# Performance work log

Hardware: AMD Instinct MI355X
Metric: run time of the kernel (lower is better)

Reference implementation:

```python
import jax, jax.numpy as jnp
import numpy as np

B, N, P_CTR, K = 16, 2048, 256, 32
H, W = 24, 80
INFEA = 64
MLP = [64, 128, 128, 256]
DIST = 0.5
EPS = 1e-5


def setup_inputs() -> dict:
    key = jax.random.key(0)
    ks = jax.random.split(key, 12)
    inp = {}
    inp['pc'] = jax.random.normal(ks[0], (B, 3, N), jnp.float32)
    inp['feat'] = jax.random.normal(ks[1], (B, INFEA, N), jnp.float32)
    inp['img1'] = jax.random.normal(ks[2], (B, MLP[0], H, W), jnp.float32)
    inp['img2'] = jax.random.normal(ks[3], (B, MLP[1], H, W), jnp.float32)
    inp['P'] = jax.random.normal(ks[4], (B, 3, 4), jnp.float32)
    inp['query_v1'] = jax.random.randint(ks[5], (B, N), 0, H * W, dtype=jnp.int32)
    inp['new_pc'] = jax.random.normal(ks[6], (B, 3, P_CTR), jnp.float32)
    dims = [INFEA + 3] + MLP  # conv chain: 67->64->128->128->256, 1x1 convs, no bias
    for i in range(4):
        fan_in = dims[i]
        inp[f'w{i+1}'] = jax.random.normal(ks[7 + i], (dims[i + 1], dims[i]), jnp.float32) * np.sqrt(2.0 / fan_in)
        inp[f'g{i+1}'] = jnp.ones((dims[i + 1],), jnp.float32)   # BN gamma, init 1
        inp[f'b{i+1}'] = jnp.zeros((dims[i + 1],), jnp.float32)  # BN beta, init 0
    return inp


def query_depth_point(pc, new_pc, dist, k):
    # depth (z-axis) ball query: pc (B,3,N), new_pc (B,3,P) -> idx (B,P,k) int32, num (B,P)
    dz = jnp.abs(pc[:, 2, None, :] - new_pc[:, 2, :, None])  # (B,P,N)
    mask = dz < dist
    num = jnp.sum(mask, axis=-1).astype(jnp.int32)           # neighbor count per center
    # stable argsort of ~mask puts valid indices first, in ascending original order
    order = jnp.argsort(jnp.logical_not(mask), axis=-1, stable=True)
    idx = order[..., :k]
    slot_valid = jnp.arange(k)[None, None, :] < jnp.minimum(num, k)[..., None]
    idx = jnp.where(slot_valid, idx, idx[..., :1])           # pad with first valid index
    return idx.astype(jnp.int32), num


def gather_ch(x, idx):
    # x (B,C,M), idx (B,L) -> (B,C,L)
    return jnp.take_along_axis(x, idx[:, None, :], axis=2)


def conv_bn_relu(x, w, g, b):
    # 1x1 conv (no bias) + BatchNorm2d (training-mode batch stats) + ReLU
    y = jnp.einsum('oc,bcnk->bonk', w, x)
    m = jnp.mean(y, axis=(0, 2, 3), keepdims=True)
    v = jnp.var(y, axis=(0, 2, 3), keepdims=True)
    y = (y - m) * jax.lax.rsqrt(v + EPS)
    y = y * g[None, :, None, None] + b[None, :, None, None]
    return jax.nn.relu(y)


def reference(pc, feat, img1, img2, P, query_v1, new_pc,
              w1, g1, b1, w2, g2, b2, w3, g3, b3, w4, g4, b4):
    idx, num = query_depth_point(pc, new_pc, DIST, K)       # (B,P,K), (B,P)
    idx_flat = idx.reshape(B, P_CTR * K)
    idx_rgb = jnp.take_along_axis(query_v1, idx_flat, axis=1)  # (B,P*K) pixel ids

    grouped_pc = gather_ch(pc, idx_flat).reshape(B, 3, P_CTR, K) - new_pc[:, :, :, None]
    grouped_feat = gather_ch(feat, idx_flat).reshape(B, INFEA, P_CTR, K)
    rgb1 = gather_ch(img1.reshape(B, MLP[0], H * W), idx_rgb).reshape(B, MLP[0], P_CTR, K)
    rgb2 = gather_ch(img2.reshape(B, MLP[1], H * W), idx_rgb).reshape(B, MLP[1], P_CTR, K)

    grouped = jnp.concatenate([grouped_pc, grouped_feat], axis=1)  # (B,67,P,K)
    pf = conv_bn_relu(grouped, w1, g1, b1)                         # (B,64,P,K)
    f1 = jnp.concatenate([pf, rgb1], axis=1)                       # (B,128,P,K)
    pf = conv_bn_relu(pf, w2, g2, b2)                              # (B,128,P,K)
    f2 = jnp.concatenate([pf, rgb2], axis=1)                       # (B,256,P,K)
    pf = conv_bn_relu(pf, w3, g3, b3)
    pf = conv_bn_relu(pf, w4, g4, b4)                              # (B,256,P,K)
    out = jnp.concatenate([f1, f2, pf], axis=1)                    # (B,640,P,K)
    valid = (num > 0).reshape(B, 1, P_CTR, 1).astype(out.dtype)
    return out * valid
```

## Files before the change

kernel.cpp:

```cpp
#include <hip/hip_runtime.h>
#include <hip/hip_fp16.h>

#define BB 16
#define NN 2048
#define PC 256
#define KK 32
#define HWS 1920
#define PT (BB*PC*KK)
#define EPSF 1e-5f

#define CH_IDXR 256
#define CH_IDX  257
#define CH_VAL  258
#define CH_FT   356
#define STATS_OFF ((size_t)259 << 13)

typedef _Float16 f16x8 __attribute__((ext_vector_type(8)));
typedef float    f32x4 __attribute__((ext_vector_type(4)));

__device__ __forceinline__ unsigned packh2(float lo, float hi) {
  unsigned a = (unsigned)__half_as_ushort(__float2half(lo));
  unsigned b = (unsigned)__half_as_ushort(__float2half(hi));
  return a | (b << 16);
}
__device__ __forceinline__ float h2lo(unsigned u) {
  return __half2float(__ushort_as_half((unsigned short)(u & 0xffffu)));
}
__device__ __forceinline__ float h2hi(unsigned u) {
  return __half2float(__ushort_as_half((unsigned short)(u >> 16)));
}

__global__ __launch_bounds__(256,2) void k_prep(
    const float* __restrict__ feat, float* out)
{
  __shared__ float tile[64][261];
  int tid = threadIdx.x;
  int b = blockIdx.x >> 3, n0 = (blockIdx.x & 7) << 8;
  #pragma unroll 8
  for (int c = 0; c < 64; c++)
    tile[c][tid] = feat[((size_t)b*64 + c)*NN + n0 + tid];
  __syncthreads();
  unsigned* ftw = (unsigned*)out + (((size_t)b*640 + CH_FT)<<13);
  #pragma unroll
  for (int e = tid; e < 256*32; e += 256) {
    int q = e & 31, nl = e >> 5;
    ftw[(size_t)(n0 + nl)*32 + q] = packh2(tile[2*q][nl], tile[2*q+1][nl]);
  }
}

template<bool WSC>
__global__ __launch_bounds__(256) void k_idx(
    const float* __restrict__ pc, const float* __restrict__ npc,
    const int* __restrict__ qv1, float* out, int* __restrict__ wsi)
{
  __shared__ int slots[4][KK];
  int tid = threadIdx.x;
  if (blockIdx.x < 5) {
    int i = blockIdx.x*256 + tid;
    if (i < 1152) out[STATS_OFF + i] = 0.0f;
  }
  int wl = tid >> 6, lane = tid & 63;
  int w = blockIdx.x*4 + wl;
  int b = w >> 8, p = w & 255;
  if (lane == 0) slots[wl][0] = 0;
  float zc = npc[(b*3+2)*PC + p];
  const float* pz = pc + ((size_t)b*3+2)*NN;
  int num = 0;
  for (int ci=0; ci<NN/64; ci++) {
    int n = ci*64 + lane;
    bool m = fabsf(pz[n] - zc) < 0.5f;
    unsigned long long mk = __ballot(m);
    if (m) {
      int rank = num + __popcll(mk & ((1ull<<lane)-1ull));
      if (rank < KK) slots[wl][rank] = n;
    }
    num += __popcll(mk);
  }
  __syncthreads();
  if (lane < KK) {
    int nj = (lane < num) ? slots[wl][lane] : slots[wl][0];
    size_t col = (size_t)p*KK + lane;
    int enc = (num > 0) ? qv1[b*NN + nj] : -1;
    ((int*)out)[(((size_t)b*640 + CH_IDX )<<13) + col] = nj;
    ((int*)out)[(((size_t)b*640 + CH_IDXR)<<13) + col] = enc;
    if constexpr (WSC) wsi[(size_t)b*8192 + col] = enc;
  }
  if (lane == 0)
    out[(((size_t)b*640 + CH_VAL)<<13) + (size_t)p*KK] = (num > 0) ? 1.0f : 0.0f;
}

#define THR 512
template<int CIN, int CINP, int COUT, int BOCH, int WVP, int WVO, int WFP, int WFO,
         int XMODE, int XBASE, int YMODE, int YBASE, int STIN, int STOUT,
         int SWZ, int QR, int PFB>
__global__ __launch_bounds__(THR,4) void k_mfma(
    const float* __restrict__ pc, const float* __restrict__ npc,
    const float* __restrict__ feat, const float* __restrict__ W,
    const float* __restrict__ g, const float* __restrict__ bv,
    float* out)
{
  __shared__ __align__(16) _Float16 xs[128*QR*2];
  __shared__ __align__(16) _Float16 ws[BOCH*QR*2];
  __shared__ float scs[128], shs[128];
  __shared__ int   idxl[128];
  __shared__ float redu[WVP*BOCH*2];

  int tid = threadIdx.x;
  int ptile = blockIdx.x;
  int b = ptile >> 6;
  int col0 = (ptile & 63) << 7;
  int och0 = blockIdx.y * BOCH;

  unsigned* xsw = (unsigned*)xs;
  unsigned* wsw = (unsigned*)ws;

  for (int e = tid; e < BOCH*QR; e += THR) {
    int o = e / QR, cq = e - o*QR;
    int c0 = 2*cq;
    float v0, v1;
    if constexpr (XMODE == 0) {
      int r0 = (c0   < 64) ? c0 + 3   : c0 - 64;
      int r1 = (c0+1 < 64) ? c0 + 4   : c0 + 1 - 64;
      v0 = (c0   < CIN) ? W[(size_t)(och0+o)*CIN + r0] : 0.f;
      v1 = (c0+1 < CIN) ? W[(size_t)(och0+o)*CIN + r1] : 0.f;
    } else {
      v0 = (c0   < CIN) ? W[(size_t)(och0+o)*CIN + c0]     : 0.f;
      v1 = (c0+1 < CIN) ? W[(size_t)(och0+o)*CIN + c0 + 1] : 0.f;
    }
    wsw[o*QR + cq] = packh2(v0, v1);
  }
  if constexpr (XMODE == 0) {
    if (tid < 128)
      idxl[tid] = ((const int*)out)[(((size_t)b*640 + CH_IDX)<<13) + col0 + tid];
  } else {
    const float* stin = out + STATS_OFF + STIN;
    for (int c = tid; c < CIN; c += THR) {
      float m   = stin[c] * (1.0f/PT);
      float var = stin[CIN+c]*(1.0f/PT) - m*m;
      float s = rsqrtf(var + EPSF) * g[c];
      scs[c] = s; shs[c] = bv[c] - m*s;
    }
  }
  __syncthreads();

  if constexpr (XMODE == 0) {
    constexpr int QG = CINP/2;
    const unsigned* ftw = (const unsigned*)out + (((size_t)b*640 + CH_FT)<<13);
    for (int e = tid; e < QG*128; e += THR) {
      int q = e % QG, pos = e / QG;
      int n = idxl[pos];
      unsigned u;
      if (q < 32) {
        u = ftw[(size_t)n*32 + q];
      } else if (q == 32) {
        int pcol = (col0 + pos) >> 5;
        float vx = pc[((size_t)b*3+0)*NN + n] - npc[(b*3+0)*PC + pcol];
        float vy = pc[((size_t)b*3+1)*NN + n] - npc[(b*3+1)*PC + pcol];
        u = packh2(vx, vy);
      } else if (q == 33) {
        int pcol = (col0 + pos) >> 5;
        float vz = pc[((size_t)b*3+2)*NN + n] - npc[(b*3+2)*PC + pcol];
        u = packh2(vz, 0.f);
      } else {
        u = 0u;
      }
      int qs = (((q>>2) ^ ((pos>>2) & SWZ)) << 2) | (q & 3);
      xsw[pos*QR + qs] = u;
    }
  } else {
    constexpr int QG = CIN/2;
    for (int e = tid; e < QG*32; e += THR) {
      int q = e >> 5, pg = e & 31;
      uint4 u = *(const uint4*)&((const unsigned*)out)[(((size_t)b*640 + XBASE + q)<<13) + col0 + pg*4];
      float s0 = scs[2*q], h0 = shs[2*q], s1 = scs[2*q+1], h1 = shs[2*q+1];
      unsigned uu[4] = {u.x, u.y, u.z, u.w};
      float lo_a[4], hi_a[4];
      #pragma unroll
      for (int j = 0; j < 4; j++) {
        float lo = fmaxf(fmaf(h2lo(uu[j]), s0, h0), 0.f);
        float hi = fmaxf(fmaf(h2hi(uu[j]), s1, h1), 0.f);
        lo_a[j] = lo; hi_a[j] = hi;
        int p = pg*4 + j;
        xsw[p*QR + ((((q>>2) ^ ((p>>2) & SWZ)) << 2) | (q & 3))] = packh2(lo, hi);
      }
      if constexpr (PFB >= 0) {
        float vv = out[(((size_t)b*640 + CH_VAL)<<13) + col0 + ((pg >> 3) << 5)];
        float4 L = {lo_a[0]*vv, lo_a[1]*vv, lo_a[2]*vv, lo_a[3]*vv};
        float4 Hh = {hi_a[0]*vv, hi_a[1]*vv, hi_a[2]*vv, hi_a[3]*vv};
        size_t pb = (((size_t)b*640 + PFB + 2*q)<<13) + col0 + pg*4;
        *(float4*)&out[pb]              = L;
        *(float4*)&out[pb + (1<<13)]    = Hh;
      }
    }
  }
  __syncthreads();

  int wv = tid >> 6, lane = tid & 63;
  int wp = wv % WVP, wo = wv / WVP;
  int lr = lane & 15, lg = lane >> 4;
  int prow0 = wp*(WFP*16), orow0 = wo*(WFO*16);

  f32x4 acc[WFP][WFO];
  const f32x4 zero4 = {0.f, 0.f, 0.f, 0.f};
  #pragma unroll
  for (int fp = 0; fp < WFP; fp++)
    #pragma unroll
    for (int fo = 0; fo < WFO; fo++) acc[fp][fo] = zero4;

  #pragma unroll
  for (int kc = 0; kc < CINP/32; kc++) {
    f16x8 af[WFP], bf[WFO];
    #pragma unroll
    for (int fp = 0; fp < WFP; fp++) {
      int row = prow0 + fp*16 + lr;
      int qb = (kc*4 + lg) ^ ((row>>2) & SWZ);
      af[fp] = *(const f16x8*)&xs[row*(QR*2) + qb*8];
    }
    #pragma unroll
    for (int fo = 0; fo < WFO; fo++) {
      int orow = orow0 + fo*16 + lr;
      bf[fo] = *(const f16x8*)&ws[orow*(QR*2) + kc*32 + lg*8];
    }
    #pragma unroll
    for (int fp = 0; fp < WFP; fp++)
      #pragma unroll
      for (int fo = 0; fo < WFO; fo++)
        acc[fp][fo] = __builtin_amdgcn_mfma_f32_16x16x32_f16(af[fp], bf[fo], acc[fp][fo], 0, 0, 0);
  }

  if constexpr (YMODE == 0) {
    #pragma unroll
    for (int fp = 0; fp < WFP; fp++) {
      int pos = col0 + prow0 + fp*16 + lg*4;
      #pragma unroll
      for (int fo = 0; fo < WFO; fo++) {
        int ochg = och0 + orow0 + fo*16 + lr;
        *(f32x4*)&out[(((size_t)b*640 + YBASE + ochg)<<13) + pos] = acc[fp][fo];
      }
    }
  } else {
    #pragma unroll
    for (int fp = 0; fp < WFP; fp++) {
      int pos = col0 + prow0 + fp*16 + lg*4;
      #pragma unroll
      for (int fo = 0; fo < WFO; fo++) {
        float pr0 = __shfl_xor(acc[fp][fo][0], 1);
        float pr1 = __shfl_xor(acc[fp][fo][1], 1);
        float pr2 = __shfl_xor(acc[fp][fo][2], 1);
        float pr3 = __shfl_xor(acc[fp][fo][3], 1);
        if (!(lane & 1)) {
          uint4 u;
          u.x = packh2(acc[fp][fo][0], pr0);
          u.y = packh2(acc[fp][fo][1], pr1);
          u.z = packh2(acc[fp][fo][2], pr2);
          u.w = packh2(acc[fp][fo][3], pr3);
          int qrow = (och0 + orow0 + fo*16 + lr) >> 1;
          *(uint4*)&((unsigned*)out)[(((size_t)b*640 + YBASE + qrow)<<13) + pos] = u;
        }
      }
    }
  }

  #pragma unroll
  for (int fo = 0; fo < WFO; fo++) {
    float s = 0.f, q2 = 0.f;
    #pragma unroll
    for (int fp = 0; fp < WFP; fp++)
      #pragma unroll
      for (int r = 0; r < 4; r++) { float v = acc[fp][fo][r]; s += v; q2 += v*v; }
    s  += __shfl_down(s, 32);  s  += __shfl_down(s, 16);
    q2 += __shfl_down(q2, 32); q2 += __shfl_down(q2, 16);
    if (lane < 16) {
      int oloc = orow0 + fo*16 + lane;
      redu[(wp*BOCH + oloc)*2]     = s;
      redu[(wp*BOCH + oloc)*2 + 1] = q2;
    }
  }
  __syncthreads();
  float* stg = out + STATS_OFF + STOUT;
  for (int i = tid; i < BOCH; i += THR) {
    float ss = 0.f, qq = 0.f;
    #pragma unroll
    for (int p = 0; p < WVP; p++) { ss += redu[(p*BOCH + i)*2]; qq += redu[(p*BOCH + i)*2 + 1]; }
    atomicAdd(&stg[och0 + i], ss);
    atomicAdd(&stg[COUT + och0 + i], qq);
  }
}

__global__ __launch_bounds__(256) void k_norm4(
    const float* __restrict__ g, const float* __restrict__ bv, float* out)
{
  __shared__ float sc[256], sh[256];
  int tid = threadIdx.x;
  const float* stin = out + STATS_OFF + 640;
  {
    float m   = stin[tid] * (1.0f/PT);
    float var = stin[256+tid]*(1.0f/PT) - m*m;
    float s = rsqrtf(var + EPSF) * g[tid];
    sc[tid] = s; sh[tid] = bv[tid] - m*s;
  }
  __syncthreads();
  int pos = blockIdx.x*256 + tid;
  int b = pos >> 13, rem = pos & 8191;
  float v = out[(((size_t)b*640 + CH_VAL)<<13) + (rem & ~31)];
  const unsigned* srcp = (const unsigned*)out + (((size_t)b*640 + 512)<<13) + rem;
  float* dstp = out + (((size_t)b*640 + 384)<<13) + rem;
  unsigned u[64];
  #pragma unroll
  for (int qi = 0; qi < 64; qi++) u[qi] = srcp[(size_t)(64+qi)<<13];
  #pragma unroll 8
  for (int qi = 0; qi < 64; qi++) {
    unsigned w = srcp[(size_t)qi<<13];
    dstp[(size_t)(2*qi)<<13]   = fmaxf(fmaf(h2lo(w), sc[2*qi],   sh[2*qi]),   0.f) * v;
    dstp[(size_t)(2*qi+1)<<13] = fmaxf(fmaf(h2hi(w), sc[2*qi+1], sh[2*qi+1]), 0.f) * v;
  }
  #pragma unroll 8
  for (int qi = 0; qi < 64; qi++) {
    dstp[(size_t)(128+2*qi)<<13]   = fmaxf(fmaf(h2lo(u[qi]), sc[128+2*qi],   sh[128+2*qi]),   0.f) * v;
    dstp[(size_t)(128+2*qi+1)<<13] = fmaxf(fmaf(h2hi(u[qi]), sc[128+2*qi+1], sh[128+2*qi+1]), 0.f) * v;
  }
}

__global__ __launch_bounds__(256) void k_rgb_lds(
    const float* __restrict__ img1, const float* __restrict__ img2,
    const int* __restrict__ wsi, float* out)
{
  __shared__ float ls[4][HWS];
  int tid = threadIdx.x;
  int b = blockIdx.x / 96, r = blockIdx.x % 96;
  int gq = r >> 1, half = r & 1;
  int gc0 = gq * 4;
  for (int e = tid; e < 4*(HWS/4); e += 256) {
    int c = e / (HWS/4), off = e % (HWS/4);
    int gc = gc0 + c;
    const float* src = (gc < 64) ? img1 + ((size_t)b*64 + gc)*HWS
                                 : img2 + ((size_t)b*128 + (gc-64))*HWS;
    *(float4*)&ls[c][off*4] = *(const float4*)&src[off*4];
  }
  __syncthreads();
  const int* idr = wsi + (size_t)b*8192;
  for (int pp = half*4096 + tid; pp < (half+1)*4096; pp += 256) {
    int enc = idr[pp];
    float v = (enc >= 0) ? 1.0f : 0.0f;
    int ir  = (enc >= 0) ? enc : 0;
    #pragma unroll
    for (int c = 0; c < 4; c++) {
      int gc = gc0 + c;
      int dch = (gc < 64) ? 64 + gc : 256 + (gc - 64);
      out[(((size_t)b*640 + dch)<<13) + pp] = ls[c][ir] * v;
    }
  }
}

__global__ __launch_bounds__(256) void k_rgb_fb(
    const float* __restrict__ img1, const float* __restrict__ img2, float* out)
{
  int tid = threadIdx.x;
  int pos = blockIdx.x*256 + tid;
  int b = pos >> 13, rem = pos & 8191;
  int enc = ((const int*)out)[(((size_t)b*640 + CH_IDXR)<<13) + rem];
  float v  = (enc >= 0) ? 1.0f : 0.0f;
  int  ir  = (enc >= 0) ? enc : 0;
  size_t o1 = (((size_t)b*640 + 64)<<13) + rem;
  const float* i1 = img1 + (size_t)b*64*HWS + ir;
  #pragma unroll 8
  for (int c=0;c<64;c++) out[o1 + ((size_t)c<<13)] = i1[(size_t)c*HWS] * v;
  size_t o2 = (((size_t)b*640 + 256)<<13) + rem;
  const float* i2 = img2 + (size_t)b*128*HWS + ir;
  #pragma unroll 8
  for (int c=0;c<128;c++) out[o2 + ((size_t)c<<13)] = i2[(size_t)c*HWS] * v;
}

extern "C" void kernel_launch(void* const* d_in, const int* in_sizes, int n_in,
                              void* d_out, int out_size, void* d_ws, size_t ws_size,
                              hipStream_t stream)
{
  const float* pc   = (const float*)d_in[0];
  const float* feat = (const float*)d_in[1];
  const float* img1 = (const float*)d_in[2];
  const float* img2 = (const float*)d_in[3];
  const int*   qv1  = (const int*)d_in[5];
  const float* npc  = (const float*)d_in[6];
  const float* w1 = (const float*)d_in[7];
  const float* g1 = (const float*)d_in[8];
  const float* b1 = (const float*)d_in[9];
  const float* w2 = (const float*)d_in[10];
  const float* g2 = (const float*)d_in[11];
  const float* b2 = (const float*)d_in[12];
  const float* w3 = (const float*)d_in[13];
  const float* g3 = (const float*)d_in[14];
  const float* b3 = (const float*)d_in[15];
  const float* w4 = (const float*)d_in[16];
  const float* g4 = (const float*)d_in[17];
  const float* b4 = (const float*)d_in[18];
  float* out = (float*)d_out;
  int*  wsi = (int*)d_ws;
  const bool use_ws = (d_ws != nullptr) && (ws_size >= (size_t)BB*8192*4);

  k_prep <<<128,256,0,stream>>>(feat, out);
  if (use_ws) k_idx<true ><<<1024,256,0,stream>>>(pc, npc, qv1, out, wsi);
  else        k_idx<false><<<1024,256,0,stream>>>(pc, npc, qv1, out, wsi);
  k_mfma<67,96,64,64,    2,4,4,1, 0,0,   1,324, 0,0,     0,48, -1>
      <<<dim3(1024,1),THR,0,stream>>>(pc,npc,feat,w1,g1,b1,out);
  k_mfma<64,64,128,128,  2,4,4,2, 1,324, 1,260, 0,128,   7,36, 0>
      <<<dim3(1024,1),THR,0,stream>>>(pc,npc,feat,w2,g1,b1,out);
  k_mfma<128,128,128,128,2,4,4,2, 1,260, 1,64,  128,384, 7,68, 128>
      <<<dim3(1024,1),THR,0,stream>>>(pc,npc,feat,w3,g2,b2,out);
  k_mfma<128,128,256,128,2,4,4,2, 1,64,  1,512, 384,640, 7,68, -1>
      <<<dim3(1024,2),THR,0,stream>>>(pc,npc,feat,w4,g3,b3,out);
  k_norm4<<<512,256,0,stream>>>(g4,b4,out);
  if (use_ws) k_rgb_lds<<<1536,256,0,stream>>>(img1, img2, wsi, out);
  else        k_rgb_fb <<<512,256,0,stream>>>(img1, img2, out);
}
```

Baseline: 654.6 us.

## Recompute final conv layer to fuse BN-ReLU output and drop norm kernel

Layer 4 now runs twice. The first pass only accumulates batch statistics. The second recomputes the GEMM and writes the normalized, ReLU'd, validity-masked fp32 output directly, which removes the fp16 intermediate round-trip and the separate k_norm4 kernel. In addition, each MFMA block now processes two point tiles with double-buffered LDS staging, keeps the fp16 weight fragments in registers instead of LDS, and the RGB gather kernel uses 512-thread blocks covering all positions. The trade is extra GEMM compute and a second read of the layer-4 input, plus higher register pressure from the register-resident weights.

```diff
diff --git a/kernel.cpp b/kernel.cpp
--- a/kernel.cpp
+++ b/kernel.cpp
@@ -8,6 +8,7 @@
 #define HWS 1920
 #define PT (BB*PC*KK)
 #define EPSF 1e-5f
+#define THR 512
 
 #define CH_IDXR 256
 #define CH_IDX  257
@@ -89,50 +90,56 @@
     out[(((size_t)b*640 + CH_VAL)<<13) + (size_t)p*KK] = (num > 0) ? 1.0f : 0.0f;
 }
 
-#define THR 512
 template<int CIN, int CINP, int COUT, int BOCH, int WVP, int WVO, int WFP, int WFO,
          int XMODE, int XBASE, int YMODE, int YBASE, int STIN, int STOUT,
-         int SWZ, int QR, int PFB>
+         int SWZ, int QR, int PFB, int TILES>
 __global__ __launch_bounds__(THR,4) void k_mfma(
     const float* __restrict__ pc, const float* __restrict__ npc,
-    const float* __restrict__ feat, const float* __restrict__ W,
+    const float* __restrict__ W,
     const float* __restrict__ g, const float* __restrict__ bv,
+    const float* __restrict__ go, const float* __restrict__ bo,
     float* out)
 {
-  __shared__ __align__(16) _Float16 xs[128*QR*2];
-  __shared__ __align__(16) _Float16 ws[BOCH*QR*2];
+  constexpr int KC = CINP/32;
+  __shared__ __align__(16) _Float16 xs[2][128*QR*2];
   __shared__ float scs[128], shs[128];
-  __shared__ int   idxl[128];
   __shared__ float redu[WVP*BOCH*2];
 
   int tid = threadIdx.x;
-  int ptile = blockIdx.x;
-  int b = ptile >> 6;
-  int col0 = (ptile & 63) << 7;
+  int tile0 = blockIdx.x * TILES;
+  int b = tile0 >> 6;
   int och0 = blockIdx.y * BOCH;
 
-  unsigned* xsw = (unsigned*)xs;
-  unsigned* wsw = (unsigned*)ws;
-
-  for (int e = tid; e < BOCH*QR; e += THR) {
-    int o = e / QR, cq = e - o*QR;
-    int c0 = 2*cq;
-    float v0, v1;
-    if constexpr (XMODE == 0) {
-      int r0 = (c0   < 64) ? c0 + 3   : c0 - 64;
-      int r1 = (c0+1 < 64) ? c0 + 4   : c0 + 1 - 64;
-      v0 = (c0   < CIN) ? W[(size_t)(och0+o)*CIN + r0] : 0.f;
-      v1 = (c0+1 < CIN) ? W[(size_t)(och0+o)*CIN + r1] : 0.f;
-    } else {
-      v0 = (c0   < CIN) ? W[(size_t)(och0+o)*CIN + c0]     : 0.f;
-      v1 = (c0+1 < CIN) ? W[(size_t)(och0+o)*CIN + c0 + 1] : 0.f;
-    }
-    wsw[o*QR + cq] = packh2(v0, v1);
-  }
-  if constexpr (XMODE == 0) {
-    if (tid < 128)
-      idxl[tid] = ((const int*)out)[(((size_t)b*640 + CH_IDX)<<13) + col0 + tid];
-  } else {
+  int wv = tid >> 6, lane = tid & 63;
+  int wp = wv % WVP, wo = wv / WVP;
+  int lr = lane & 15, lg = lane >> 4;
+  int prow0 = wp*(WFP*16), orow0 = wo*(WFO*16);
+
+  f16x8 bfr[KC][WFO];
+  #pragma unroll
+  for (int kc = 0; kc < KC; kc++)
+    #pragma unroll
+    for (int fo = 0; fo < WFO; fo++) {
+      int orow = och0 + orow0 + fo*16 + lr;
+      f16x8 tf;
+      if constexpr (XMODE == 0) {
+        #pragma unroll
+        for (int j = 0; j < 8; j++) {
+          int c = kc*32 + lg*8 + j;
+          int r = (c < 64) ? c + 3 : (c < 67 ? c - 64 : -1);
+          tf[j] = (_Float16)((r >= 0) ? W[(size_t)orow*CIN + r] : 0.f);
+        }
+      } else {
+        const float* wr = W + (size_t)orow*CIN + kc*32 + lg*8;
+        float4 w0 = *(const float4*)wr;
+        float4 w1 = *(const float4*)(wr + 4);
+        tf[0]=(_Float16)w0.x; tf[1]=(_Float16)w0.y; tf[2]=(_Float16)w0.z; tf[3]=(_Float16)w0.w;
+        tf[4]=(_Float16)w1.x; tf[5]=(_Float16)w1.y; tf[6]=(_Float16)w1.z; tf[7]=(_Float16)w1.w;
+      }
+      bfr[kc][fo] = tf;
+    }
+
+  if constexpr (XMODE == 1) {
     const float* stin = out + STATS_OFF + STIN;
     for (int c = tid; c < CIN; c += THR) {
       float m   = stin[c] * (1.0f/PT);
@@ -141,196 +148,194 @@
       scs[c] = s; shs[c] = bv[c] - m*s;
     }
   }
+  float osc_[WFO], osh_[WFO];
+  if constexpr (YMODE == 3) {
+    const float* sto = out + STATS_OFF + STOUT;
+    #pragma unroll
+    for (int fo = 0; fo < WFO; fo++) {
+      int och = och0 + orow0 + fo*16 + lr;
+      float m   = sto[och]*(1.0f/PT);
+      float var = sto[COUT+och]*(1.0f/PT) - m*m;
+      float s = rsqrtf(var + EPSF) * go[och];
+      osc_[fo] = s; osh_[fo] = bo[och] - m*s;
+    }
+  }
   __syncthreads();
 
-  if constexpr (XMODE == 0) {
-    constexpr int QG = CINP/2;
-    const unsigned* ftw = (const unsigned*)out + (((size_t)b*640 + CH_FT)<<13);
-    for (int e = tid; e < QG*128; e += THR) {
-      int q = e % QG, pos = e / QG;
-      int n = idxl[pos];
-      unsigned u;
-      if (q < 32) {
-        u = ftw[(size_t)n*32 + q];
-      } else if (q == 32) {
-        int pcol = (col0 + pos) >> 5;
-        float vx = pc[((size_t)b*3+0)*NN + n] - npc[(b*3+0)*PC + pcol];
-        float vy = pc[((size_t)b*3+1)*NN + n] - npc[(b*3+1)*PC + pcol];
-        u = packh2(vx, vy);
-      } else if (q == 33) {
-        int pcol = (col0 + pos) >> 5;
-        float vz = pc[((size_t)b*3+2)*NN + n] - npc[(b*3+2)*PC + pcol];
-        u = packh2(vz, 0.f);
-      } else {
-        u = 0u;
-      }
-      int qs = (((q>>2) ^ ((pos>>2) & SWZ)) << 2) | (q & 3);
-      xsw[pos*QR + qs] = u;
-    }
-  } else {
-    constexpr int QG = CIN/2;
-    for (int e = tid; e < QG*32; e += THR) {
-      int q = e >> 5, pg = e & 31;
-      uint4 u = *(const uint4*)&((const unsigned*)out)[(((size_t)b*640 + XBASE + q)<<13) + col0 + pg*4];
-      float s0 = scs[2*q], h0 = shs[2*q], s1 = scs[2*q+1], h1 = shs[2*q+1];
-      unsigned uu[4] = {u.x, u.y, u.z, u.w};
-      float lo_a[4], hi_a[4];
-      #pragma unroll
-      for (int j = 0; j < 4; j++) {
-        float lo = fmaxf(fmaf(h2lo(uu[j]), s0, h0), 0.f);
-        float hi = fmaxf(fmaf(h2hi(uu[j]), s1, h1), 0.f);
-        lo_a[j] = lo; hi_a[j] = hi;
-        int p = pg*4 + j;
-        xsw[p*QR + ((((q>>2) ^ ((p>>2) & SWZ)) << 2) | (q & 3))] = packh2(lo, hi);
-      }
-      if constexpr (PFB >= 0) {
-        float vv = out[(((size_t)b*640 + CH_VAL)<<13) + col0 + ((pg >> 3) << 5)];
-        float4 L = {lo_a[0]*vv, lo_a[1]*vv, lo_a[2]*vv, lo_a[3]*vv};
-        float4 Hh = {hi_a[0]*vv, hi_a[1]*vv, hi_a[2]*vv, hi_a[3]*vv};
-        size_t pb = (((size_t)b*640 + PFB + 2*q)<<13) + col0 + pg*4;
-        *(float4*)&out[pb]              = L;
-        *(float4*)&out[pb + (1<<13)]    = Hh;
-      }
-    }
-  }
+  auto STAGE = [&](int t) {
+    int col0t = ((tile0 + t) & 63) << 7;
+    unsigned* xw = (unsigned*)xs[t & 1];
+    if constexpr (XMODE == 0) {
+      int posl = tid & 127;
+      int qb0  = tid >> 7;
+      int n = ((const int*)out)[(((size_t)b*640 + CH_IDX)<<13) + col0t + posl];
+      const unsigned* ftw = (const unsigned*)out + (((size_t)b*640 + CH_FT)<<13);
+      int pcol = (col0t + posl) >> 5;
+      #pragma unroll
+      for (int k = 0; k < 12; k++) {
+        int q = qb0 + k*4;
+        unsigned u;
+        if (q < 32) {
+          u = ftw[(size_t)n*32 + q];
+        } else if (q == 32) {
+          float vx = pc[((size_t)b*3+0)*NN + n] - npc[(b*3+0)*PC + pcol];
+          float vy = pc[((size_t)b*3+1)*NN + n] - npc[(b*3+1)*PC + pcol];
+          u = packh2(vx, vy);
+        } else if (q == 33) {
+          float vz = pc[((size_t)b*3+2)*NN + n] - npc[(b*3+2)*PC + pcol];
+          u = packh2(vz, 0.f);
+        } else u = 0u;
+        int qs = (((q>>2) ^ ((posl>>2) & SWZ)) << 2) | (q & 3);
+        xw[posl*QR + qs] = u;
+      }
+    } else {
+      #pragma unroll
+      for (int k = 0; k < CIN/32; k++) {
+        int e = tid + k*THR;
+        int q = e >> 5, pg = e & 31;
+        uint4 u = *(const uint4*)&((const unsigned*)out)[(((size_t)b*640 + XBASE + q)<<13) + col0t + pg*4];
+        float s0 = scs[2*q], h0 = shs[2*q], s1 = scs[2*q+1], h1 = shs[2*q+1];
+        unsigned uu[4] = {u.x, u.y, u.z, u.w};
+        float lo_a[4], hi_a[4];
+        #pragma unroll
+        for (int j = 0; j < 4; j++) {
+          lo_a[j] = fmaxf(fmaf(h2lo(uu[j]), s0, h0), 0.f);
+          hi_a[j] = fmaxf(fmaf(h2hi(uu[j]), s1, h1), 0.f);
+          int p = pg*4 + j;
+          xw[p*QR + ((((q>>2) ^ ((p>>2) & SWZ)) << 2) | (q & 3))] = packh2(lo_a[j], hi_a[j]);
+        }
+        if constexpr (PFB >= 0) {
+          float vv = out[(((size_t)b*640 + CH_VAL)<<13) + col0t + ((pg >> 3) << 5)];
+          float4 L  = {lo_a[0]*vv, lo_a[1]*vv, lo_a[2]*vv, lo_a[3]*vv};
+          float4 Hh = {hi_a[0]*vv, hi_a[1]*vv, hi_a[2]*vv, hi_a[3]*vv};
+          size_t pb = (((size_t)b*640 + PFB + 2*q)<<13) + col0t + pg*4;
+          *(float4*)&out[pb]           = L;
+          *(float4*)&out[pb + (1<<13)] = Hh;
+        }
+      }
+    }
+  };
+
+  STAGE(0);
   __syncthreads();
 
-  int wv = tid >> 6, lane = tid & 63;
-  int wp = wv % WVP, wo = wv / WVP;
-  int lr = lane & 15, lg = lane >> 4;
-  int prow0 = wp*(WFP*16), orow0 = wo*(WFO*16);
-
-  f32x4 acc[WFP][WFO];
-  const f32x4 zero4 = {0.f, 0.f, 0.f, 0.f};
+  float ssum[WFO], ssq[WFO];
   #pragma unroll
-  for (int fp = 0; fp < WFP; fp++)
-    #pragma unroll
-    for (int fo = 0; fo < WFO; fo++) acc[fp][fo] = zero4;
+  for (int fo = 0; fo < WFO; fo++) { ssum[fo] = 0.f; ssq[fo] = 0.f; }
 
   #pragma unroll
-  for (int kc = 0; kc < CINP/32; kc++) {
-    f16x8 af[WFP], bf[WFO];
-    #pragma unroll
-    for (int fp = 0; fp < WFP; fp++) {
-      int row = prow0 + fp*16 + lr;
-      int qb = (kc*4 + lg) ^ ((row>>2) & SWZ);
-      af[fp] = *(const f16x8*)&xs[row*(QR*2) + qb*8];
-    }
+  for (int t = 0; t < TILES; t++) {
+    int col0t = ((tile0 + t) & 63) << 7;
+    const _Float16* xb = xs[t & 1];
+
+    f32x4 acc[WFP][WFO];
+    const f32x4 zero4 = {0.f, 0.f, 0.f, 0.f};
+    #pragma unroll
+    for (int fp = 0; fp < WFP; fp++)
+      #pragma unroll
+      for (int fo = 0; fo < WFO; fo++) acc[fp][fo] = zero4;
+
+    #pragma unroll
+    for (int kc = 0; kc < KC; kc++) {
+      f16x8 af[WFP];
+      #pragma unroll
+      for (int fp = 0; fp < WFP; fp++) {
+        int row = prow0 + fp*16 + lr;
+        int qb = (kc*4 + lg) ^ ((row>>2) & SWZ);
+        af[fp] = *(const f16x8*)&xb[row*(QR*2) + qb*8];
+      }
+      #pragma unroll
+      for (int fp = 0; fp < WFP; fp++)
+        #pragma unroll
+        for (int fo = 0; fo < WFO; fo++)
+          acc[fp][fo] = __builtin_amdgcn_mfma_f32_16x16x32_f16(af[fp], bfr[kc][fo], acc[fp][fo], 0, 0, 0);
+    }
+
+    if constexpr (YMODE == 1) {
+      #pragma unroll
+      for (int fp = 0; fp < WFP; fp++) {
+        int pos = col0t + prow0 + fp*16 + lg*4;
+        #pragma unroll
+        for (int fo = 0; fo < WFO; fo++) {
+          float pr0 = __shfl_xor(acc[fp][fo][0], 1);
+          float pr1 = __shfl_xor(acc[fp][fo][1], 1);
+          float pr2 = __shfl_xor(acc[fp][fo][2], 1);
+          float pr3 = __shfl_xor(acc[fp][fo][3], 1);
+          if (!(lane & 1)) {
+            uint4 u;
+            u.x = packh2(acc[fp][fo][0], pr0); u.y = packh2(acc[fp][fo][1], pr1);
+            u.z = packh2(acc[fp][fo][2], pr2); u.w = packh2(acc[fp][fo][3], pr3);
+            int qrow = (och0 + orow0 + fo*16 + lr) >> 1;
+            *(uint4*)&((unsigned*)out)[(((size_t)b*640 + YBASE + qrow)<<13) + pos] = u;
+          }
+        }
+      }
+    } else if constexpr (YMODE == 3) {
+      #pragma unroll
+      for (int fp = 0; fp < WFP; fp++) {
+        int pos = col0t + prow0 + fp*16 + lg*4;
+        float v = out[(((size_t)b*640 + CH_VAL)<<13) + (pos & ~31)];
+        #pragma unroll
+        for (int fo = 0; fo < WFO; fo++) {
+          int och = och0 + orow0 + fo*16 + lr;
+          f32x4 wv;
+          #pragma unroll
+          for (int r = 0; r < 4; r++)
+            wv[r] = fmaxf(fmaf(acc[fp][fo][r], osc_[fo], osh_[fo]), 0.f) * v;
+          *(f32x4*)&out[(((size_t)b*640 + YBASE + och)<<13) + pos] = wv;
+        }
+      }
+    }
+
+    if constexpr (YMODE != 3) {
+      #pragma unroll
+      for (int fo = 0; fo < WFO; fo++)
+        #pragma unroll
+        for (int fp = 0; fp < WFP; fp++)
+          #pragma unroll
+          for (int r = 0; r < 4; r++) {
+            float v = acc[fp][fo][r];
+            ssum[fo] += v; ssq[fo] += v*v;
+          }
+    }
+
+    if (t + 1 < TILES) STAGE(t + 1);
+    __syncthreads();
+  }
+
+  if constexpr (YMODE != 3) {
     #pragma unroll
     for (int fo = 0; fo < WFO; fo++) {
-      int orow = orow0 + fo*16 + lr;
-      bf[fo] = *(const f16x8*)&ws[orow*(QR*2) + kc*32 + lg*8];
-    }
-    #pragma unroll
-    for (int fp = 0; fp < WFP; fp++)
-      #pragma unroll
-      for (int fo = 0; fo < WFO; fo++)
-        acc[fp][fo] = __builtin_amdgcn_mfma_f32_16x16x32_f16(af[fp], bf[fo], acc[fp][fo], 0, 0, 0);
-  }
-
-  if constexpr (YMODE == 0) {
-    #pragma unroll
-    for (int fp = 0; fp < WFP; fp++) {
-      int pos = col0 + prow0 + fp*16 + lg*4;
-      #pragma unroll
-      for (int fo = 0; fo < WFO; fo++) {
-        int ochg = och0 + orow0 + fo*16 + lr;
-        *(f32x4*)&out[(((size_t)b*640 + YBASE + ochg)<<13) + pos] = acc[fp][fo];
-      }
-    }
-  } else {
-    #pragma unroll
-    for (int fp = 0; fp < WFP; fp++) {
-      int pos = col0 + prow0 + fp*16 + lg*4;
-      #pragma unroll
-      for (int fo = 0; fo < WFO; fo++) {
-        float pr0 = __shfl_xor(acc[fp][fo][0], 1);
-        float pr1 = __shfl_xor(acc[fp][fo][1], 1);
-        float pr2 = __shfl_xor(acc[fp][fo][2], 1);
-        float pr3 = __shfl_xor(acc[fp][fo][3], 1);
-        if (!(lane & 1)) {
-          uint4 u;
-          u.x = packh2(acc[fp][fo][0], pr0);
-          u.y = packh2(acc[fp][fo][1], pr1);
-          u.z = packh2(acc[fp][fo][2], pr2);
-          u.w = packh2(acc[fp][fo][3], pr3);
-          int qrow = (och0 + orow0 + fo*16 + lr) >> 1;
-          *(uint4*)&((unsigned*)out)[(((size_t)b*640 + YBASE + qrow)<<13) + pos] = u;
-        }
-      }
-    }
-  }
-
-  #pragma unroll
-  for (int fo = 0; fo < WFO; fo++) {
-    float s = 0.f, q2 = 0.f;
-    #pragma unroll
-    for (int fp = 0; fp < WFP; fp++)
-      #pragma unroll
-      for (int r = 0; r < 4; r++) { float v = acc[fp][fo][r]; s += v; q2 += v*v; }
-    s  += __shfl_down(s, 32);  s  += __shfl_down(s, 16);
-    q2 += __shfl_down(q2, 32); q2 += __shfl_down(q2, 16);
-    if (lane < 16) {
-      int oloc = orow0 + fo*16 + lane;
-      redu[(wp*BOCH + oloc)*2]     = s;
-      redu[(wp*BOCH + oloc)*2 + 1] = q2;
-    }
-  }
-  __syncthreads();
-  float* stg = out + STATS_OFF + STOUT;
-  for (int i = tid; i < BOCH; i += THR) {
-    float ss = 0.f, qq = 0.f;
-    #pragma unroll
-    for (int p = 0; p < WVP; p++) { ss += redu[(p*BOCH + i)*2]; qq += redu[(p*BOCH + i)*2 + 1]; }
-    atomicAdd(&stg[och0 + i], ss);
-    atomicAdd(&stg[COUT + och0 + i], qq);
-  }
-}
-
-__global__ __launch_bounds__(256) void k_norm4(
-    const float* __restrict__ g, const float* __restrict__ bv, float* out)
-{
-  __shared__ float sc[256], sh[256];
-  int tid = threadIdx.x;
-  const float* stin = out + STATS_OFF + 640;
-  {
-    float m   = stin[tid] * (1.0f/PT);
-    float var = stin[256+tid]*(1.0f/PT) - m*m;
-    float s = rsqrtf(var + EPSF) * g[tid];
-    sc[tid] = s; sh[tid] = bv[tid] - m*s;
-  }
-  __syncthreads();
-  int pos = blockIdx.x*256 + tid;
-  int b = pos >> 13, rem = pos & 8191;
-  float v = out[(((size_t)b*640 + CH_VAL)<<13) + (rem & ~31)];
-  const unsigned* srcp = (const unsigned*)out + (((size_t)b*640 + 512)<<13) + rem;
-  float* dstp = out + (((size_t)b*640 + 384)<<13) + rem;
-  unsigned u[64];
-  #pragma unroll
-  for (int qi = 0; qi < 64; qi++) u[qi] = srcp[(size_t)(64+qi)<<13];
-  #pragma unroll 8
-  for (int qi = 0; qi < 64; qi++) {
-    unsigned w = srcp[(size_t)qi<<13];
-    dstp[(size_t)(2*qi)<<13]   = fmaxf(fmaf(h2lo(w), sc[2*qi],   sh[2*qi]),   0.f) * v;
-    dstp[(size_t)(2*qi+1)<<13] = fmaxf(fmaf(h2hi(w), sc[2*qi+1], sh[2*qi+1]), 0.f) * v;
-  }
-  #pragma unroll 8
-  for (int qi = 0; qi < 64; qi++) {
-    dstp[(size_t)(128+2*qi)<<13]   = fmaxf(fmaf(h2lo(u[qi]), sc[128+2*qi],   sh[128+2*qi]),   0.f) * v;
-    dstp[(size_t)(128+2*qi+1)<<13] = fmaxf(fmaf(h2hi(u[qi]), sc[128+2*qi+1], sh[128+2*qi+1]), 0.f) * v;
-  }
-}
-
-__global__ __launch_bounds__(256) void k_rgb_lds(
+      float s = ssum[fo], q2 = ssq[fo];
+      s  += __shfl_down(s, 32);  s  += __shfl_down(s, 16);
+      q2 += __shfl_down(q2, 32); q2 += __shfl_down(q2, 16);
+      if (lane < 16) {
+        int oloc = orow0 + fo*16 + lane;
+        redu[(wp*BOCH + oloc)*2]     = s;
+        redu[(wp*BOCH + oloc)*2 + 1] = q2;
+      }
+    }
+    __syncthreads();
+    float* stg = out + STATS_OFF + STOUT;
+    for (int i = tid; i < BOCH; i += THR) {
+      float ss = 0.f, qq = 0.f;
+      #pragma unroll
+      for (int p = 0; p < WVP; p++) { ss += redu[(p*BOCH + i)*2]; qq += redu[(p*BOCH + i)*2 + 1]; }
+      atomicAdd(&stg[och0 + i], ss);
+      atomicAdd(&stg[COUT + och0 + i], qq);
+    }
+  }
+}
+
+__global__ __launch_bounds__(512) void k_rgb_lds(
     const float* __restrict__ img1, const float* __restrict__ img2,
     const int* __restrict__ wsi, float* out)
 {
   __shared__ float ls[4][HWS];
   int tid = threadIdx.x;
-  int b = blockIdx.x / 96, r = blockIdx.x % 96;
-  int gq = r >> 1, half = r & 1;
+  int b = blockIdx.x / 48, gq = blockIdx.x % 48;
   int gc0 = gq * 4;
-  for (int e = tid; e < 4*(HWS/4); e += 256) {
+  for (int e = tid; e < 4*(HWS/4); e += 512) {
     int c = e / (HWS/4), off = e % (HWS/4);
     int gc = gc0 + c;
     const float* src = (gc < 64) ? img1 + ((size_t)b*64 + gc)*HWS
@@ -339,16 +344,14 @@
   }
   __syncthreads();
   const int* idr = wsi + (size_t)b*8192;
-  for (int pp = half*4096 + tid; pp < (half+1)*4096; pp += 256) {
+  int dch0 = (gc0 < 64) ? 64 + gc0 : 256 + (gc0 - 64);
+  for (int pp = tid; pp < 8192; pp += 512) {
     int enc = idr[pp];
     float v = (enc >= 0) ? 1.0f : 0.0f;
     int ir  = (enc >= 0) ? enc : 0;
     #pragma unroll
-    for (int c = 0; c < 4; c++) {
-      int gc = gc0 + c;
-      int dch = (gc < 64) ? 64 + gc : 256 + (gc - 64);
-      out[(((size_t)b*640 + dch)<<13) + pp] = ls[c][ir] * v;
-    }
+    for (int c = 0; c < 4; c++)
+      out[(((size_t)b*640 + dch0 + c)<<13) + pp] = ls[c][ir] * v;
   }
 }
 
@@ -400,15 +403,16 @@
   k_prep <<<128,256,0,stream>>>(feat, out);
   if (use_ws) k_idx<true ><<<1024,256,0,stream>>>(pc, npc, qv1, out, wsi);
   else        k_idx<false><<<1024,256,0,stream>>>(pc, npc, qv1, out, wsi);
-  k_mfma<67,96,64,64,    2,4,4,1, 0,0,   1,324, 0,0,     0,48, -1>
-      <<<dim3(1024,1),THR,0,stream>>>(pc,npc,feat,w1,g1,b1,out);
-  k_mfma<64,64,128,128,  2,4,4,2, 1,324, 1,260, 0,128,   7,36, 0>
-      <<<dim3(1024,1),THR,0,stream>>>(pc,npc,feat,w2,g1,b1,out);
-  k_mfma<128,128,128,128,2,4,4,2, 1,260, 1,64,  128,384, 7,68, 128>
-      <<<dim3(1024,1),THR,0,stream>>>(pc,npc,feat,w3,g2,b2,out);
-  k_mfma<128,128,256,128,2,4,4,2, 1,64,  1,512, 384,640, 7,68, -1>
-      <<<dim3(1024,2),THR,0,stream>>>(pc,npc,feat,w4,g3,b3,out);
-  k_norm4<<<512,256,0,stream>>>(g4,b4,out);
-  if (use_ws) k_rgb_lds<<<1536,256,0,stream>>>(img1, img2, wsi, out);
+  k_mfma<67,96,64,64,    2,4,4,1, 0,0,   1,324, 0,0,     0,48, -1,2>
+      <<<dim3(512,1),THR,0,stream>>>(pc,npc,w1,g1,b1,g1,b1,out);
+  k_mfma<64,64,128,128,  2,4,4,2, 1,324, 1,260, 0,128,   7,36, 0,2>
+      <<<dim3(512,1),THR,0,stream>>>(pc,npc,w2,g1,b1,g1,b1,out);
+  k_mfma<128,128,128,128,2,4,4,2, 1,260, 1,64,  128,384, 7,68, 128,2>
+      <<<dim3(512,1),THR,0,stream>>>(pc,npc,w3,g2,b2,g2,b2,out);
+  k_mfma<128,128,256,128,2,4,4,2, 1,64,  2,0,   384,640, 7,68, -1,2>
+      <<<dim3(512,2),THR,0,stream>>>(pc,npc,w4,g3,b3,g3,b3,out);
+  k_mfma<128,128,256,128,2,4,4,2, 1,64,  3,384, 384,640, 7,68, -1,2>
+      <<<dim3(512,2),THR,0,stream>>>(pc,npc,w4,g3,b3,g4,b4,out);
+  if (use_ws) k_rgb_lds<<<768,512,0,stream>>>(img1, img2, wsi, out);
   else        k_rgb_fb <<<512,256,0,stream>>>(img1, img2, out);
 }
```

Result: faster. 579.9 us (-11.4%).
